# Kernel optimization log

Hardware: AMD Instinct MI355X
Metric: run time of the kernel (lower is better)

Reference implementation:

```python
import jax, jax.numpy as jnp
import numpy as np

B, D, L = 16384, 1024, 3


def setup_inputs() -> dict:
    key = jax.random.key(0)
    kx, kw, kb = jax.random.split(key, 3)
    # xavier_normal for a (D, 1) tensor: std = sqrt(2 / (D + 1))
    std = float(np.sqrt(2.0 / (D + 1)))
    x = jax.random.normal(kx, (B, D), dtype=jnp.float32)
    weights = jax.random.normal(kw, (L, D), dtype=jnp.float32) * std
    bias = jax.random.normal(kb, (L, D), dtype=jnp.float32) * std
    return {"x": x, "weights": weights, "bias": bias}


def reference(x, weights, bias):
    # DCN cross layer: xl_{t+1} = x0 * (xl_t . w_t) + b_t + xl_t
    # (identical math to matmul(x0 xl^T, w) + b + xl, without the [B,D,D] intermediate)
    x0 = x

    def layer(xl, wb):
        w, b = wb  # [D], [D]
        s = xl @ w  # [B] scaled dot-product reduction
        xl_new = x0 * s[:, None] + b + xl  # [B, D]
        return xl_new, None

    out, _ = jax.lax.scan(layer, x, (weights, bias))
    return out
```

## Files before the change

kernel.cpp:

```cpp
#include <hip/hip_runtime.h>


#define CN_B 16384
#define CN_D 1024
#define CN_L 3

__global__ __launch_bounds__(256) void crossnet_kernel(
    const float* __restrict__ x,
    const float* __restrict__ w,
    const float* __restrict__ bias,
    float* __restrict__ out) {
  const int row  = blockIdx.x;
  const int tid  = threadIdx.x;
  const int wave = tid >> 6;
  const int lane = tid & 63;

  const float4* xrow = reinterpret_cast<const float4*>(x + (size_t)row * CN_D);
  float4 x0 = xrow[tid];
  float4 xl = x0;

  __shared__ float red[4];

  #pragma unroll
  for (int l = 0; l < CN_L; ++l) {
    const float4 wl = reinterpret_cast<const float4*>(w    + l * CN_D)[tid];
    const float4 bl = reinterpret_cast<const float4*>(bias + l * CN_D)[tid];

    float p = xl.x * wl.x + xl.y * wl.y + xl.z * wl.z + xl.w * wl.w;

    #pragma unroll
    for (int off = 32; off > 0; off >>= 1)
      p += __shfl_down(p, off, 64);

    if (lane == 0) red[wave] = p;
    __syncthreads();

    const float s = red[0] + red[1] + red[2] + red[3];

    xl.x = x0.x * s + bl.x + xl.x;
    xl.y = x0.y * s + bl.y + xl.y;
    xl.z = x0.z * s + bl.z + xl.z;
    xl.w = x0.w * s + bl.w + xl.w;

    __syncthreads();
  }

  reinterpret_cast<float4*>(out + (size_t)row * CN_D)[tid] = xl;
}

extern "C" void kernel_launch(void* const* d_in, const int* in_sizes, int n_in,
                              void* d_out, int out_size, void* d_ws, size_t ws_size,
                              hipStream_t stream) {
  const float* x    = (const float*)d_in[0];
  const float* w    = (const float*)d_in[1];
  const float* bias = (const float*)d_in[2];
  float* out        = (float*)d_out;

  crossnet_kernel<<<CN_B, 256, 0, stream>>>(x, w, bias, out);
}
```

Measured before the change: 30.12 us.

## Map one wavefront per row and drop shared-memory block reductions

Each 64-lane wave now owns a full row, with four float4 elements per lane, so the dot-product reduction is done entirely with xor shuffles. This removes the shared-memory partial sums and both __syncthreads per layer. Blocks now process four rows each and the grid shrinks accordingly. Register use per thread grows because each lane keeps four float4 x0 and xl values plus the weights and biases.

```diff
diff --git a/kernel.cpp b/kernel.cpp
--- a/kernel.cpp
+++ b/kernel.cpp
@@ -4,48 +4,63 @@
 #define CN_B 16384
 #define CN_D 1024
 #define CN_L 3
+#define ROWS_PER_BLOCK 4
 
-__global__ __launch_bounds__(256) void crossnet_kernel(
+__global__ __launch_bounds__(256, 4) void crossnet_kernel(
     const float* __restrict__ x,
     const float* __restrict__ w,
     const float* __restrict__ bias,
     float* __restrict__ out) {
-  const int row  = blockIdx.x;
   const int tid  = threadIdx.x;
   const int wave = tid >> 6;
   const int lane = tid & 63;
+  const int row  = blockIdx.x * ROWS_PER_BLOCK + wave;
 
   const float4* xrow = reinterpret_cast<const float4*>(x + (size_t)row * CN_D);
-  float4 x0 = xrow[tid];
-  float4 xl = x0;
-
-  __shared__ float red[4];
+  float4 x0[4], xl[4];
+  #pragma unroll
+  for (int k = 0; k < 4; ++k) {
+    x0[k] = xrow[k * 64 + lane];
+    xl[k] = x0[k];
+  }
 
   #pragma unroll
   for (int l = 0; l < CN_L; ++l) {
-    const float4 wl = reinterpret_cast<const float4*>(w    + l * CN_D)[tid];
-    const float4 bl = reinterpret_cast<const float4*>(bias + l * CN_D)[tid];
+    const float4* wrow = reinterpret_cast<const float4*>(w    + l * CN_D);
+    const float4* brow = reinterpret_cast<const float4*>(bias + l * CN_D);
+    float4 wl[4], bl[4];
+    #pragma unroll
+    for (int k = 0; k < 4; ++k) {
+      wl[k] = wrow[k * 64 + lane];
+      bl[k] = brow[k * 64 + lane];
+    }
 
-    float p = xl.x * wl.x + xl.y * wl.y + xl.z * wl.z + xl.w * wl.w;
+    float p = 0.0f;
+    #pragma unroll
+    for (int k = 0; k < 4; ++k) {
+      p += xl[k].x * wl[k].x;
+      p += xl[k].y * wl[k].y;
+      p += xl[k].z * wl[k].z;
+      p += xl[k].w * wl[k].w;
+    }
 
     #pragma unroll
     for (int off = 32; off > 0; off >>= 1)
-      p += __shfl_down(p, off, 64);
+      p += __shfl_xor(p, off, 64);
 
-    if (lane == 0) red[wave] = p;
-    __syncthreads();
-
-    const float s = red[0] + red[1] + red[2] + red[3];
-
-    xl.x = x0.x * s + bl.x + xl.x;
-    xl.y = x0.y * s + bl.y + xl.y;
-    xl.z = x0.z * s + bl.z + xl.z;
-    xl.w = x0.w * s + bl.w + xl.w;
-
-    __syncthreads();
+    #pragma unroll
+    for (int k = 0; k < 4; ++k) {
+      xl[k].x = x0[k].x * p + bl[k].x + xl[k].x;
+      xl[k].y = x0[k].y * p + bl[k].y + xl[k].y;
+      xl[k].z = x0[k].z * p + bl[k].z + xl[k].z;
+      xl[k].w = x0[k].w * p + bl[k].w + xl[k].w;
+    }
   }
 
-  reinterpret_cast<float4*>(out + (size_t)row * CN_D)[tid] = xl;
+  float4* orow = reinterpret_cast<float4*>(out + (size_t)row * CN_D);
+  #pragma unroll
+  for (int k = 0; k < 4; ++k)
+    orow[k * 64 + lane] = xl[k];
 }
 
 extern "C" void kernel_launch(void* const* d_in, const int* in_sizes, int n_in,
@@ -56,5 +71,5 @@
   const float* bias = (const float*)d_in[2];
   float* out        = (float*)d_out;
 
-  crossnet_kernel<<<CN_B, 256, 0, stream>>>(x, w, bias, out);
+  crossnet_kernel<<<CN_B / ROWS_PER_BLOCK, 256, 0, stream>>>(x, w, bias, out);
 }
```

Result: no change. 30.00 us (-0.4%).
